# Kernel optimization log

Hardware: AMD Instinct MI355X
Metric: run time of the kernel (lower is better)

The kernel has to match this reference:

```python
import jax, jax.numpy as jnp
import numpy as np

QLEN, MLEN, BSZ, DMODEL, NHEAD, DHEAD, DFF = 1024, 1024, 4, 1024, 16, 64, 4096
KLEN = QLEN + MLEN


def _layernorm(x, g, b, eps=1e-5):
    mu = jnp.mean(x, axis=-1, keepdims=True)
    var = jnp.var(x, axis=-1, keepdims=True)
    return (x - mu) * jax.lax.rsqrt(var + eps) * g + b


def _rel_shift(x):
    # x: [qlen, klen, bsz, nhead] -- Transformer-XL shift trick
    q, k, b, n = x.shape
    x = jnp.pad(x, ((0, 0), (1, 0), (0, 0), (0, 0)))  # [q, k+1, b, n]
    x = x.reshape(k + 1, q, b, n)[1:]
    return x.reshape(q, k, b, n)


def setup_inputs() -> dict:
    key = jax.random.key(0)
    ks = jax.random.split(key, 16)
    s = 0.02
    inp = {
        "word_embed": jax.random.normal(ks[0], (QLEN, BSZ, DMODEL), jnp.float32),
        "pos_embed": jax.random.normal(ks[1], (KLEN, DMODEL), jnp.float32),
        "bias_q": jax.random.normal(ks[2], (NHEAD, DHEAD), jnp.float32) * s,
        "bias_k": jax.random.normal(ks[3], (NHEAD, DHEAD), jnp.float32) * s,
        "memories": jax.random.normal(ks[4], (MLEN, BSZ, DMODEL), jnp.float32),
        "W_qkv": jax.random.normal(ks[5], (DMODEL, 3 * NHEAD * DHEAD), jnp.float32) * s,
        "W_r": jax.random.normal(ks[6], (DMODEL, NHEAD * DHEAD), jnp.float32) * s,
        "W_o": jax.random.normal(ks[7], (NHEAD * DHEAD, DMODEL), jnp.float32) * s,
        "ln1_g": jnp.ones((DMODEL,), jnp.float32),
        "ln1_b": jnp.zeros((DMODEL,), jnp.float32),
        "W_ff1": jax.random.normal(ks[8], (DMODEL, DFF), jnp.float32) * s,
        "b_ff1": jnp.zeros((DFF,), jnp.float32),
        "W_ff2": jax.random.normal(ks[9], (DFF, DMODEL), jnp.float32) * s,
        "b_ff2": jnp.zeros((DMODEL,), jnp.float32),
        "ln2_g": jnp.ones((DMODEL,), jnp.float32),
        "ln2_b": jnp.zeros((DMODEL,), jnp.float32),
    }
    # causal mask with memory: position i may attend to j <= i + MLEN; True = masked
    i = jnp.arange(QLEN)[:, None]
    j = jnp.arange(KLEN)[None, :]
    inp["attention_mask"] = j > (i + MLEN)
    return inp


def reference(word_embed, pos_embed, bias_q, bias_k, attention_mask, memories,
              W_qkv, W_r, W_o, ln1_g, ln1_b, W_ff1, b_ff1, W_ff2, b_ff2, ln2_g, ln2_b):
    scale = 1.0 / np.sqrt(DHEAD)
    cat = jnp.concatenate([memories, word_embed], axis=0)  # [klen, b, d]
    w_heads = cat @ W_qkv  # [klen, b, 3*n*dh]
    q, k, v = jnp.split(w_heads, 3, axis=-1)
    q = q[-QLEN:].reshape(QLEN, BSZ, NHEAD, DHEAD)
    k = k.reshape(KLEN, BSZ, NHEAD, DHEAD)
    v = v.reshape(KLEN, BSZ, NHEAD, DHEAD)
    r = (pos_embed @ W_r).reshape(KLEN, NHEAD, DHEAD)

    AC = jnp.einsum('ibnd,jbnd->ijbn', q + bias_q, k)          # content term
    BD = jnp.einsum('ibnd,jnd->ijbn', q + bias_k, r)           # position term
    BD = _rel_shift(BD)
    score = (AC + BD) * scale
    score = jnp.where(attention_mask[:, :, None, None], -1e30, score)
    prob = jax.nn.softmax(score, axis=1)
    attn_vec = jnp.einsum('ijbn,jbnd->ibnd', prob, v).reshape(QLEN, BSZ, NHEAD * DHEAD)
    attn_out = attn_vec @ W_o
    out = _layernorm(word_embed + attn_out, ln1_g, ln1_b)       # post-LN (pre_lnorm=False)

    core = jax.nn.relu(out @ W_ff1 + b_ff1) @ W_ff2 + b_ff2
    return _layernorm(out + core, ln2_g, ln2_b)
```

## Files before the change

kernel.cpp:

```cpp
#include <hip/hip_runtime.h>


typedef __bf16 bf16x8 __attribute__((ext_vector_type(8)));
typedef float f32x4 __attribute__((ext_vector_type(4)));

#define DEVI __device__ __forceinline__

DEVI unsigned short f2bf(float f) {
  union { float f; unsigned int u; } v;
  v.f = f;
  unsigned int u = v.u;
  u += 0x7fffu + ((u >> 16) & 1u);
  return (unsigned short)(u >> 16);
}

DEVI void load16(const unsigned short* g, unsigned short* l) {
  __builtin_amdgcn_global_load_lds(
      (const __attribute__((address_space(1))) unsigned int*)g,
      (__attribute__((address_space(3))) unsigned int*)l, 16, 0, 0);
}

__global__ __launch_bounds__(256) void cvt_all_kernel(
    const float* __restrict__ mem, const float* __restrict__ we,
    const float* __restrict__ pe, unsigned short* __restrict__ catb,
    unsigned short* __restrict__ posb) {
  const int b = blockIdx.x;
  const float* in;
  unsigned short* out;
  int idx;
  if (b < 4096) {
    in = mem; out = catb; idx = b;
  } else if (b < 8192) {
    in = we; out = catb + (size_t)4096 * 1024; idx = b - 4096;
  } else {
    in = pe; out = posb; idx = b - 8192;
  }
  const size_t i = ((size_t)idx * 256 + threadIdx.x) * 4;
  float4 v = *(const float4*)(in + i);
  ushort4 o;
  o.x = f2bf(v.x);
  o.y = f2bf(v.y);
  o.z = f2bf(v.z);
  o.w = f2bf(v.w);
  *(ushort4*)(out + i) = o;
}

__global__ __launch_bounds__(256) void transpose_all_kernel(
    const float* __restrict__ Wqkv, const float* __restrict__ Wr,
    const float* __restrict__ Wo, const float* __restrict__ Wff1,
    const float* __restrict__ Wff2, unsigned short* __restrict__ Tqkv,
    unsigned short* __restrict__ Tr, unsigned short* __restrict__ To,
    unsigned short* __restrict__ Tff1, unsigned short* __restrict__ Tff2) {
  __shared__ unsigned short t[64][72];
  const int b = blockIdx.x;
  const float* in;
  unsigned short* out;
  int ntx, R, C, local;
  if (b < 768) {
    in = Wqkv; out = Tqkv; ntx = 48; R = 1024; C = 3072; local = b;
  } else if (b < 1024) {
    in = Wr; out = Tr; ntx = 16; R = 1024; C = 1024; local = b - 768;
  } else if (b < 1280) {
    in = Wo; out = To; ntx = 16; R = 1024; C = 1024; local = b - 1024;
  } else if (b < 2304) {
    in = Wff1; out = Tff1; ntx = 64; R = 1024; C = 4096; local = b - 1280;
  } else {
    in = Wff2; out = Tff2; ntx = 16; R = 4096; C = 1024; local = b - 2304;
  }
  const int r0 = (local / ntx) * 64, c0 = (local % ntx) * 64;
  const int tid = threadIdx.x;
#pragma unroll
  for (int it = 0; it < 4; ++it) {
    int f = tid + 256 * it;
    int r = f >> 4;
    int c4 = (f & 15) << 2;
    float4 v = *(const float4*)(in + (size_t)(r0 + r) * C + c0 + c4);
    t[c4 + 0][r] = f2bf(v.x);
    t[c4 + 1][r] = f2bf(v.y);
    t[c4 + 2][r] = f2bf(v.z);
    t[c4 + 3][r] = f2bf(v.w);
  }
  __syncthreads();
#pragma unroll
  for (int it = 0; it < 4; ++it) {
    int f = tid + 256 * it;
    int cc = f >> 4;
    int r4 = (f & 15) << 2;
    ushort4 o;
    o.x = t[cc][r4 + 0];
    o.y = t[cc][r4 + 1];
    o.z = t[cc][r4 + 2];
    o.w = t[cc][r4 + 3];
    *(ushort4*)(out + (size_t)(c0 + cc) * R + r0 + r4) = o;
  }
}

struct GemmArgs {
  const unsigned short* A;
  const unsigned short* Bt;
  int Ks;
  int M, N, K;
  const float* p0;
  const float* p1;
  const float* resid;
  float* outF;
  unsigned short* o0;
  unsigned short* o1;
  unsigned short* o2;
  unsigned short* o3;
  int relu;
  int partial;
};

constexpr int BM = 128, BK = 64;

template <int EPI, int WN = 4>
__global__ __launch_bounds__(256, 4) void gemm_kernel(GemmArgs ga) {
  constexpr int BN_ = WN * 32;
  __shared__ __align__(16) unsigned short As[BM * BK];
  __shared__ __align__(16) unsigned short Bs[BN_ * BK];

  int m0, n0;
  if constexpr (EPI == 0) {
    const int flat = blockIdx.x;
    int mt_, nt_;
    if (flat < 1024) {
      mt_ = flat >> 4;
      nt_ = 8 + (flat & 15);
    } else {
      const int f2 = flat - 1024;
      mt_ = 32 + (f2 >> 3);
      nt_ = f2 & 7;
    }
    m0 = mt_ * 128;
    n0 = nt_ * 128;
  } else {
    n0 = blockIdx.x * BN_;
    m0 = blockIdx.y * BM;
  }
  const int bz = blockIdx.z;
  const int tid = threadIdx.x;
  const int lane = tid & 63;
  const int wv = tid >> 6;
  const int l15 = lane & 15;
  const int quad = lane >> 4;
  const int wm = wv & 1, wn = wv >> 1;
  const int K = ga.K;
  const int Ks = ga.Ks;
  const int r8 = lane >> 3;
  const int sc = (lane & 7) ^ r8;

  const f32x4 fzero = {0.f, 0.f, 0.f, 0.f};
  f32x4 acc[4][WN];
#pragma unroll
  for (int i = 0; i < 4; ++i)
#pragma unroll
    for (int j = 0; j < WN; ++j) acc[i][j] = fzero;

  const unsigned short* Ab =
      ga.A + (size_t)(m0 + 32 * wv + r8) * K + sc * 8 + (size_t)bz * Ks;
  const unsigned short* Bb =
      ga.Bt + (size_t)(n0 + (BN_ / 4) * wv + r8) * K + sc * 8 + (size_t)bz * Ks;
  const int h7 = l15 & 7;

  for (int k0 = 0; k0 < Ks; k0 += BK) {
    __syncthreads();
#pragma unroll
    for (int it = 0; it < 4; ++it)
      load16(Ab + (size_t)(8 * it) * K + k0, &As[(32 * wv + 8 * it) * 64]);
#pragma unroll
    for (int it = 0; it < BN_ / 32; ++it)
      load16(Bb + (size_t)(8 * it) * K + k0, &Bs[((BN_ / 4) * wv + 8 * it) * 64]);
    __syncthreads();
#pragma unroll
    for (int ks = 0; ks < 2; ++ks) {
      bf16x8 af[4], bg[WN];
#pragma unroll
      for (int mt = 0; mt < 4; ++mt)
        af[mt] = *(const bf16x8*)&As[(wm * 64 + mt * 16 + l15) * 64 +
                                     (((ks * 4 + quad) ^ h7) * 8)];
#pragma unroll
      for (int nt = 0; nt < WN; ++nt)
        bg[nt] = *(const bf16x8*)&Bs[(wn * (WN * 16) + nt * 16 + l15) * 64 +
                                     (((ks * 4 + quad) ^ h7) * 8)];
#pragma unroll
      for (int mt = 0; mt < 4; ++mt)
#pragma unroll
        for (int nt = 0; nt < WN; ++nt)
          acc[mt][nt] =
              __builtin_amdgcn_mfma_f32_16x16x32_bf16(af[mt], bg[nt], acc[mt][nt], 0, 0, 0);
    }
  }

#pragma unroll
  for (int mt = 0; mt < 4; ++mt) {
#pragma unroll
    for (int nt = 0; nt < WN; ++nt) {
#pragma unroll
      for (int r = 0; r < 4; ++r) {
        const int row = m0 + wm * 64 + mt * 16 + quad * 4 + r;
        const int col = n0 + wn * (WN * 16) + nt * 16 + l15;
        float val = acc[mt][nt][r];
        if constexpr (EPI == 0) {
          const int seq = row >> 2, b = row & 3;
          if (col < 1024) {
            if (seq >= 1024) {
              const int nh = col >> 6, d = col & 63;
              const size_t o = ((size_t)((b * 16 + nh) * 1024 + (seq - 1024))) * 64 + d;
              ga.o0[o] = f2bf(val + ga.p0[col]);
              ga.o1[o] = f2bf(val + ga.p1[col]);
            }
          } else if (col < 2048) {
            const int c = col - 1024, nh = c >> 6, d = c & 63, bn = b * 16 + nh;
            const size_t o = (size_t)bn * 131072 +
                             (size_t)(((seq >> 4) * 2 + (d >> 5)) * 512) +
                             ((((d >> 3) & 3) * 16 + (seq & 15)) * 8) + (d & 7);
            ga.o2[o] = f2bf(val);
          } else {
            const int c = col - 2048, nh = c >> 6, d = c & 63, bn = b * 16 + nh;
            const size_t o = (size_t)bn * 131072 + (size_t)((seq >> 7) * 8192) +
                             ((((seq >> 5) & 3) * 4 + (d >> 4)) * 512) +
                             ((((seq >> 3) & 3) * 16 + (d & 15)) * 8) + (seq & 7);
            ga.o3[o] = f2bf(val);
          }
        } else if constexpr (EPI == 1) {
          const int nh = col >> 6, d = col & 63, t = row;
          const size_t o = (size_t)nh * 131072 +
                           (size_t)(((t >> 4) * 2 + (d >> 5)) * 512) +
                           ((((d >> 3) & 3) * 16 + (t & 15)) * 8) + (d & 7);
          ga.o0[o] = f2bf(val);
        } else {
          if (ga.partial) {
            ga.outF[(size_t)bz * ((size_t)ga.M * ga.N) + (size_t)row * ga.N + col] = val;
          } else {
            if (ga.p0) val += ga.p0[col];
            if (ga.resid) val += ga.resid[(size_t)row * ga.N + col];
            if (ga.relu) val = fmaxf(val, 0.f);
            if (ga.outF) ga.outF[(size_t)row * ga.N + col] = val;
            if (ga.o0) ga.o0[(size_t)row * ga.N + col] = f2bf(val);
          }
        }
      }
    }
  }
}

constexpr int P_LD = 136;
constexpr float CEXP = 0.18033688f;

__global__ __launch_bounds__(256, 4) void attn_kernel(
    const unsigned short* __restrict__ QQ, const unsigned short* __restrict__ QK,
    const unsigned short* __restrict__ Kf, const unsigned short* __restrict__ Vf,
    const unsigned short* __restrict__ Rf, unsigned short* __restrict__ AVb) {
  __shared__ __align__(16) unsigned short p_s[4][16 * P_LD];

  const int tid = threadIdx.x;
  const int lane = tid & 63;
  const int wv = tid >> 6;
  const int l15 = lane & 15;
  const int quad = lane >> 4;
  const int bn = blockIdx.x;
  const int iw = (blockIdx.y * 4 + wv) * 16;
  const int nh = bn & 15;
  const int bb = bn >> 4;
  unsigned short* pw = &p_s[wv][0];

  const unsigned short* kf = Kf + (size_t)bn * 131072;
  const unsigned short* vf = Vf + (size_t)bn * 131072;
  const unsigned short* rf = Rf + (size_t)nh * 131072;

  const size_t qoff = (size_t)bn * (1024 * 64) + (size_t)(iw + l15) * 64;
  const bf16x8 qq0 = *(const bf16x8*)(QQ + qoff + quad * 8);
  const bf16x8 qq1 = *(const bf16x8*)(QQ + qoff + 32 + quad * 8);
  const bf16x8 qk0 = *(const bf16x8*)(QK + qoff + quad * 8);
  const bf16x8 qk1 = *(const bf16x8*)(QK + qoff + 32 + quad * 8);

  const f32x4 fzero = {0.f, 0.f, 0.f, 0.f};
  f32x4 o_acc[4];
#pragma unroll
  for (int i = 0; i < 4; ++i) o_acc[i] = fzero;
  float lsum[4] = {0.f, 0.f, 0.f, 0.f};

  const int lane8 = lane * 8;
  const int jmax = iw + 15 + 1024;
  for (int j0 = 0; j0 <= jmax; j0 += 128) {
    const int t16b = (j0 >> 4) + 63 - (iw >> 4);
    f32x4 bd[9];
#pragma unroll
    for (int ct = 0; ct < 9; ++ct) {
      int tg = t16b + ct;
      tg = (tg < 127) ? tg : 127;
      const unsigned short* rb = rf + (size_t)(tg * 1024) + lane8;
      bf16x8 b0 = *(const bf16x8*)rb;
      bf16x8 b1 = *(const bf16x8*)(rb + 512);
      f32x4 c = fzero;
      c = __builtin_amdgcn_mfma_f32_16x16x32_bf16(qk0, b0, c, 0, 0, 0);
      c = __builtin_amdgcn_mfma_f32_16x16x32_bf16(qk1, b1, c, 0, 0, 0);
      bd[ct] = c;
    }

    const int ntb = j0 >> 4;
    f32x4 sv[8];
#pragma unroll
    for (int nt = 0; nt < 8; ++nt) {
      const unsigned short* kb = kf + (size_t)((ntb + nt) * 1024) + lane8;
      bf16x8 b0 = *(const bf16x8*)kb;
      bf16x8 b1 = *(const bf16x8*)(kb + 512);
      f32x4 c = fzero;
      c = __builtin_amdgcn_mfma_f32_16x16x32_bf16(qq0, b0, c, 0, 0, 0);
      c = __builtin_amdgcn_mfma_f32_16x16x32_bf16(qq1, b1, c, 0, 0, 0);
      sv[nt] = c;
    }

#pragma unroll
    for (int r = 0; r < 4; ++r) {
      const int il = quad * 4 + r;
      const int u = l15 + 15 - il;
      const int srcl = (lane & 48) | (u & 15);
      float w[9];
#pragma unroll
      for (int ct = 0; ct < 9; ++ct) w[ct] = __shfl(bd[ct][r], srcl, 64);
      const int ig = iw + il;
#pragma unroll
      for (int nt = 0; nt < 8; ++nt) {
        const float bdv = (u & 16) ? w[nt + 1] : w[nt];
        const int jg = j0 + nt * 16 + l15;
        float p = exp2f((sv[nt][r] + bdv) * CEXP);
        p = (jg > ig + 1024) ? 0.f : p;
        lsum[r] += p;
        pw[il * P_LD + nt * 16 + l15] = f2bf(p);
      }
    }

    const unsigned short* vb = vf + (size_t)((j0 >> 7) * 8192) + lane8;
#pragma unroll
    for (int ks = 0; ks < 4; ++ks) {
      bf16x8 ap = *(const bf16x8*)&pw[l15 * P_LD + ks * 32 + quad * 8];
#pragma unroll
      for (int nto = 0; nto < 4; ++nto) {
        bf16x8 bv = *(const bf16x8*)(vb + (ks * 4 + nto) * 512);
        o_acc[nto] = __builtin_amdgcn_mfma_f32_16x16x32_bf16(ap, bv, o_acc[nto], 0, 0, 0);
      }
    }
  }

  float linv[4];
#pragma unroll
  for (int r = 0; r < 4; ++r) {
    float l = lsum[r];
    l += __shfl_xor(l, 1, 64);
    l += __shfl_xor(l, 2, 64);
    l += __shfl_xor(l, 4, 64);
    l += __shfl_xor(l, 8, 64);
    linv[r] = 1.f / l;
  }
#pragma unroll
  for (int nto = 0; nto < 4; ++nto) {
#pragma unroll
    for (int r = 0; r < 4; ++r) {
      const int ig = iw + quad * 4 + r;
      const int d = nto * 16 + l15;
      const float val = o_acc[nto][r] * linv[r];
      AVb[(size_t)(ig * 4 + bb) * 1024 + nh * 64 + d] = f2bf(val);
    }
  }
}

__global__ __launch_bounds__(256) void ln_sum_kernel(
    const float* __restrict__ x0, const float* __restrict__ x1,
    const float* __restrict__ bias, const float* __restrict__ resid,
    const float* __restrict__ g, const float* __restrict__ bta,
    float* __restrict__ outF, unsigned short* __restrict__ outB) {
  const int row = blockIdx.x;
  const int tid = threadIdx.x;
  const size_t off = (size_t)row * 1024 + tid * 4;
  float4 v = *(const float4*)(x0 + off);
  const float4 w = *(const float4*)(x1 + off);
  v.x += w.x; v.y += w.y; v.z += w.z; v.w += w.w;
  if (bias) {
    const float4 b = *(const float4*)(bias + tid * 4);
    v.x += b.x; v.y += b.y; v.z += b.z; v.w += b.w;
  }
  if (resid) {
    const float4 rr = *(const float4*)(resid + off);
    v.x += rr.x; v.y += rr.y; v.z += rr.z; v.w += rr.w;
  }
  float s = v.x + v.y + v.z + v.w;
  float ss = v.x * v.x + v.y * v.y + v.z * v.z + v.w * v.w;
#pragma unroll
  for (int off2 = 1; off2 < 64; off2 <<= 1) {
    s += __shfl_xor(s, off2, 64);
    ss += __shfl_xor(ss, off2, 64);
  }
  __shared__ float red[8];
  const int wv = tid >> 6;
  if ((tid & 63) == 0) {
    red[wv] = s;
    red[4 + wv] = ss;
  }
  __syncthreads();
  s = red[0] + red[1] + red[2] + red[3];
  ss = red[4] + red[5] + red[6] + red[7];
  const float mu = s * (1.f / 1024.f);
  const float var = ss * (1.f / 1024.f) - mu * mu;
  const float rs = rsqrtf(var + 1e-5f);
  const float vv[4] = {v.x, v.y, v.z, v.w};
#pragma unroll
  for (int u = 0; u < 4; ++u) {
    const int c = tid * 4 + u;
    const float y = (vv[u] - mu) * rs * g[c] + bta[c];
    if (outF) outF[(size_t)row * 1024 + c] = y;
    if (outB) outB[(size_t)row * 1024 + c] = f2bf(y);
  }
}

extern "C" void kernel_launch(void* const* d_in, const int* in_sizes, int n_in,
                              void* d_out, int out_size, void* d_ws, size_t ws_size,
                              hipStream_t stream) {
  (void)in_sizes; (void)n_in; (void)out_size; (void)ws_size;
  const float* word_embed = (const float*)d_in[0];
  const float* pos_embed = (const float*)d_in[1];
  const float* bias_q = (const float*)d_in[2];
  const float* bias_k = (const float*)d_in[3];
  const float* memories = (const float*)d_in[4];
  const float* W_qkv = (const float*)d_in[5];
  const float* W_r = (const float*)d_in[6];
  const float* W_o = (const float*)d_in[7];
  const float* ln1_g = (const float*)d_in[8];
  const float* ln1_b = (const float*)d_in[9];
  const float* W_ff1 = (const float*)d_in[10];
  const float* b_ff1 = (const float*)d_in[11];
  const float* W_ff2 = (const float*)d_in[12];
  const float* b_ff2 = (const float*)d_in[13];
  const float* ln2_g = (const float*)d_in[14];
  const float* ln2_b = (const float*)d_in[15];
  float* out = (float*)d_out;

  char* ws = (char*)d_ws;
  unsigned short* QQ = (unsigned short*)(ws + 0);
  unsigned short* QK = (unsigned short*)(ws + 8388608);
  unsigned short* Kf = (unsigned short*)(ws + 16777216);
  unsigned short* Vf = (unsigned short*)(ws + 50331648);
  unsigned short* Rf = (unsigned short*)(ws + 67108864);
  unsigned short* AVb = (unsigned short*)(ws + 71303168);
  float* OUT1 = (float*)(ws + 96468992);
  unsigned short* OUT1b = (unsigned short*)(ws + 113246208);
  unsigned short* Wqkv_t = (unsigned short*)(ws + 121634816);
  unsigned short* Wr_t = (unsigned short*)(ws + 127926272);
  unsigned short* Wo_t = (unsigned short*)(ws + 130023424);
  unsigned short* Wff1_t = (unsigned short*)(ws + 132120576);
  unsigned short* Wff2_t = (unsigned short*)(ws + 140509184);
  unsigned short* Catb = (unsigned short*)(ws + 79691776);
  unsigned short* Posb = (unsigned short*)(ws + 96468992);
  unsigned short* H = (unsigned short*)(ws + 0);
  float* Pwo = (float*)(ws + 33554432);
  float* Pff = (float*)(ws + 50331648);

  const dim3 blk(256);

  cvt_all_kernel<<<10240, blk, 0, stream>>>(memories, word_embed, pos_embed, Catb, Posb);
  transpose_all_kernel<<<3328, blk, 0, stream>>>(W_qkv, W_r, W_o, W_ff1, W_ff2,
                                                 Wqkv_t, Wr_t, Wo_t, Wff1_t, Wff2_t);

  {
    GemmArgs a{};
    a.A = Catb;
    a.Bt = Wqkv_t;
    a.M = 8192; a.N = 3072; a.K = 1024; a.Ks = 1024;
    a.p0 = bias_q; a.p1 = bias_k;
    a.o0 = QQ; a.o1 = QK; a.o2 = Kf; a.o3 = Vf;
    gemm_kernel<0><<<dim3(1280), blk, 0, stream>>>(a);
  }
  {
    GemmArgs a{};
    a.A = Posb;
    a.Bt = Wr_t;
    a.M = 2048; a.N = 1024; a.K = 1024; a.Ks = 1024;
    a.o0 = Rf;
    gemm_kernel<1, 1><<<dim3(32, 16), blk, 0, stream>>>(a);
  }

  attn_kernel<<<dim3(64, 16), blk, 0, stream>>>(QQ, QK, Kf, Vf, Rf, AVb);

  {
    GemmArgs a{};
    a.A = AVb;
    a.Bt = Wo_t;
    a.M = 4096; a.N = 1024; a.K = 1024; a.Ks = 512;
    a.outF = Pwo;
    a.partial = 1;
    gemm_kernel<2, 2><<<dim3(16, 32, 2), blk, 0, stream>>>(a);
  }
  ln_sum_kernel<<<4096, blk, 0, stream>>>(Pwo, Pwo + (size_t)4096 * 1024, nullptr,
                                          word_embed, ln1_g, ln1_b, OUT1, OUT1b);

  {
    GemmArgs a{};
    a.A = OUT1b;
    a.Bt = Wff1_t;
    a.M = 4096; a.N = 4096; a.K = 1024; a.Ks = 1024;
    a.p0 = b_ff1;
    a.relu = 1;
    a.o0 = H;
    gemm_kernel<2><<<dim3(32, 32), blk, 0, stream>>>(a);
  }
  {
    GemmArgs a{};
    a.A = H;
    a.Bt = Wff2_t;
    a.M = 4096; a.N = 1024; a.K = 4096; a.Ks = 2048;
    a.outF = Pff;
    a.partial = 1;
    gemm_kernel<2, 2><<<dim3(16, 32, 2), blk, 0, stream>>>(a);
  }
  ln_sum_kernel<<<4096, blk, 0, stream>>>(Pff, Pff + (size_t)4096 * 1024, b_ff2,
                                          OUT1, ln2_g, ln2_b, out, nullptr);
}
```

Before: 612.1 us.

## Add double-buffered LDS GEMM kernel for narrow-N GEMMs

Adds a gemm_db kernel that keeps two LDS buffers for A and B tiles and issues the next K-tile's global-to-LDS loads before computing on the current one. This needs only one barrier per iteration instead of the single-buffer load/sync/compute/sync sequence. It is used for the positional projection, the W_o GEMM and the FF2 GEMM, all of which have small N tiles. The epilogue is factored into a shared helper. Doubling LDS per block may reduce occupancy, and the in-flight loads may race with reads if the async LDS load ordering is not guaranteed.

```diff
diff --git a/kernel.cpp b/kernel.cpp
--- a/kernel.cpp
+++ b/kernel.cpp
@@ -112,6 +112,49 @@
   int partial;
 };
 
+template <int EPI>
+DEVI void epi_store(const GemmArgs& ga, int bz, int row, int col, float val) {
+  if constexpr (EPI == 0) {
+    const int seq = row >> 2, b = row & 3;
+    if (col < 1024) {
+      if (seq >= 1024) {
+        const int nh = col >> 6, d = col & 63;
+        const size_t o = ((size_t)((b * 16 + nh) * 1024 + (seq - 1024))) * 64 + d;
+        ga.o0[o] = f2bf(val + ga.p0[col]);
+        ga.o1[o] = f2bf(val + ga.p1[col]);
+      }
+    } else if (col < 2048) {
+      const int c = col - 1024, nh = c >> 6, d = c & 63, bn = b * 16 + nh;
+      const size_t o = (size_t)bn * 131072 +
+                       (size_t)(((seq >> 4) * 2 + (d >> 5)) * 512) +
+                       ((((d >> 3) & 3) * 16 + (seq & 15)) * 8) + (d & 7);
+      ga.o2[o] = f2bf(val);
+    } else {
+      const int c = col - 2048, nh = c >> 6, d = c & 63, bn = b * 16 + nh;
+      const size_t o = (size_t)bn * 131072 + (size_t)((seq >> 7) * 8192) +
+                       ((((seq >> 5) & 3) * 4 + (d >> 4)) * 512) +
+                       ((((seq >> 3) & 3) * 16 + (d & 15)) * 8) + (seq & 7);
+      ga.o3[o] = f2bf(val);
+    }
+  } else if constexpr (EPI == 1) {
+    const int nh = col >> 6, d = col & 63, t = row;
+    const size_t o = (size_t)nh * 131072 +
+                     (size_t)(((t >> 4) * 2 + (d >> 5)) * 512) +
+                     ((((d >> 3) & 3) * 16 + (t & 15)) * 8) + (d & 7);
+    ga.o0[o] = f2bf(val);
+  } else {
+    if (ga.partial) {
+      ga.outF[(size_t)bz * ((size_t)ga.M * ga.N) + (size_t)row * ga.N + col] = val;
+    } else {
+      if (ga.p0) val += ga.p0[col];
+      if (ga.resid) val += ga.resid[(size_t)row * ga.N + col];
+      if (ga.relu) val = fmaxf(val, 0.f);
+      if (ga.outF) ga.outF[(size_t)row * ga.N + col] = val;
+      if (ga.o0) ga.o0[(size_t)row * ga.N + col] = f2bf(val);
+    }
+  }
+}
+
 constexpr int BM = 128, BK = 64;
 
 template <int EPI, int WN = 4>
@@ -193,56 +236,97 @@
   }
 
 #pragma unroll
-  for (int mt = 0; mt < 4; ++mt) {
-#pragma unroll
-    for (int nt = 0; nt < WN; ++nt) {
+  for (int mt = 0; mt < 4; ++mt)
+#pragma unroll
+    for (int nt = 0; nt < WN; ++nt)
 #pragma unroll
       for (int r = 0; r < 4; ++r) {
         const int row = m0 + wm * 64 + mt * 16 + quad * 4 + r;
         const int col = n0 + wn * (WN * 16) + nt * 16 + l15;
-        float val = acc[mt][nt][r];
-        if constexpr (EPI == 0) {
-          const int seq = row >> 2, b = row & 3;
-          if (col < 1024) {
-            if (seq >= 1024) {
-              const int nh = col >> 6, d = col & 63;
-              const size_t o = ((size_t)((b * 16 + nh) * 1024 + (seq - 1024))) * 64 + d;
-              ga.o0[o] = f2bf(val + ga.p0[col]);
-              ga.o1[o] = f2bf(val + ga.p1[col]);
-            }
-          } else if (col < 2048) {
-            const int c = col - 1024, nh = c >> 6, d = c & 63, bn = b * 16 + nh;
-            const size_t o = (size_t)bn * 131072 +
-                             (size_t)(((seq >> 4) * 2 + (d >> 5)) * 512) +
-                             ((((d >> 3) & 3) * 16 + (seq & 15)) * 8) + (d & 7);
-            ga.o2[o] = f2bf(val);
-          } else {
-            const int c = col - 2048, nh = c >> 6, d = c & 63, bn = b * 16 + nh;
-            const size_t o = (size_t)bn * 131072 + (size_t)((seq >> 7) * 8192) +
-                             ((((seq >> 5) & 3) * 4 + (d >> 4)) * 512) +
-                             ((((seq >> 3) & 3) * 16 + (d & 15)) * 8) + (seq & 7);
-            ga.o3[o] = f2bf(val);
-          }
-        } else if constexpr (EPI == 1) {
-          const int nh = col >> 6, d = col & 63, t = row;
-          const size_t o = (size_t)nh * 131072 +
-                           (size_t)(((t >> 4) * 2 + (d >> 5)) * 512) +
-                           ((((d >> 3) & 3) * 16 + (t & 15)) * 8) + (d & 7);
-          ga.o0[o] = f2bf(val);
-        } else {
-          if (ga.partial) {
-            ga.outF[(size_t)bz * ((size_t)ga.M * ga.N) + (size_t)row * ga.N + col] = val;
-          } else {
-            if (ga.p0) val += ga.p0[col];
-            if (ga.resid) val += ga.resid[(size_t)row * ga.N + col];
-            if (ga.relu) val = fmaxf(val, 0.f);
-            if (ga.outF) ga.outF[(size_t)row * ga.N + col] = val;
-            if (ga.o0) ga.o0[(size_t)row * ga.N + col] = f2bf(val);
-          }
-        }
+        epi_store<EPI>(ga, bz, row, col, acc[mt][nt][r]);
       }
-    }
-  }
+}
+
+template <int EPI, int WN = 2>
+__global__ __launch_bounds__(256, 4) void gemm_db(GemmArgs ga) {
+  constexpr int BN_ = WN * 32;
+  __shared__ __align__(16) unsigned short As[2][BM * BK];
+  __shared__ __align__(16) unsigned short Bs[2][BN_ * BK];
+
+  const int n0 = blockIdx.x * BN_;
+  const int m0 = blockIdx.y * BM;
+  const int bz = blockIdx.z;
+  const int tid = threadIdx.x;
+  const int lane = tid & 63;
+  const int wv = tid >> 6;
+  const int l15 = lane & 15;
+  const int quad = lane >> 4;
+  const int wm = wv & 1, wn = wv >> 1;
+  const int K = ga.K;
+  const int Ks = ga.Ks;
+  const int r8 = lane >> 3;
+  const int sc = (lane & 7) ^ r8;
+  const int h7 = l15 & 7;
+
+  const f32x4 fzero = {0.f, 0.f, 0.f, 0.f};
+  f32x4 acc[4][WN];
+#pragma unroll
+  for (int i = 0; i < 4; ++i)
+#pragma unroll
+    for (int j = 0; j < WN; ++j) acc[i][j] = fzero;
+
+  const unsigned short* Ab =
+      ga.A + (size_t)(m0 + 32 * wv + r8) * K + sc * 8 + (size_t)bz * Ks;
+  const unsigned short* Bb =
+      ga.Bt + (size_t)(n0 + (BN_ / 4) * wv + r8) * K + sc * 8 + (size_t)bz * Ks;
+
+  auto stage = [&](int k0, int bi) {
+#pragma unroll
+    for (int it = 0; it < 4; ++it)
+      load16(Ab + (size_t)(8 * it) * K + k0, &As[bi][(32 * wv + 8 * it) * 64]);
+#pragma unroll
+    for (int it = 0; it < BN_ / 32; ++it)
+      load16(Bb + (size_t)(8 * it) * K + k0, &Bs[bi][((BN_ / 4) * wv + 8 * it) * 64]);
+  };
+
+  stage(0, 0);
+  __syncthreads();
+
+  int buf = 0;
+  for (int k0 = 0; k0 < Ks; k0 += BK) {
+    if (k0 + BK < Ks) stage(k0 + BK, buf ^ 1);
+#pragma unroll
+    for (int ks = 0; ks < 2; ++ks) {
+      bf16x8 af[4], bg[WN];
+#pragma unroll
+      for (int mt = 0; mt < 4; ++mt)
+        af[mt] = *(const bf16x8*)&As[buf][(wm * 64 + mt * 16 + l15) * 64 +
+                                         (((ks * 4 + quad) ^ h7) * 8)];
+#pragma unroll
+      for (int nt = 0; nt < WN; ++nt)
+        bg[nt] = *(const bf16x8*)&Bs[buf][(wn * (WN * 16) + nt * 16 + l15) * 64 +
+                                          (((ks * 4 + quad) ^ h7) * 8)];
+#pragma unroll
+      for (int mt = 0; mt < 4; ++mt)
+#pragma unroll
+        for (int nt = 0; nt < WN; ++nt)
+          acc[mt][nt] =
+              __builtin_amdgcn_mfma_f32_16x16x32_bf16(af[mt], bg[nt], acc[mt][nt], 0, 0, 0);
+    }
+    __syncthreads();
+    buf ^= 1;
+  }
+
+#pragma unroll
+  for (int mt = 0; mt < 4; ++mt)
+#pragma unroll
+    for (int nt = 0; nt < WN; ++nt)
+#pragma unroll
+      for (int r = 0; r < 4; ++r) {
+        const int row = m0 + wm * 64 + mt * 16 + quad * 4 + r;
+        const int col = n0 + wn * (WN * 16) + nt * 16 + l15;
+        epi_store<EPI>(ga, bz, row, col, acc[mt][nt][r]);
+      }
 }
 
 constexpr int P_LD = 136;
@@ -477,7 +561,7 @@
     a.Bt = Wr_t;
     a.M = 2048; a.N = 1024; a.K = 1024; a.Ks = 1024;
     a.o0 = Rf;
-    gemm_kernel<1, 1><<<dim3(32, 16), blk, 0, stream>>>(a);
+    gemm_db<1, 1><<<dim3(32, 16), blk, 0, stream>>>(a);
   }
 
   attn_kernel<<<dim3(64, 16), blk, 0, stream>>>(QQ, QK, Kf, Vf, Rf, AVb);
@@ -489,7 +573,7 @@
     a.M = 4096; a.N = 1024; a.K = 1024; a.Ks = 512;
     a.outF = Pwo;
     a.partial = 1;
-    gemm_kernel<2, 2><<<dim3(16, 32, 2), blk, 0, stream>>>(a);
+    gemm_db<2, 2><<<dim3(16, 32, 2), blk, 0, stream>>>(a);
   }
   ln_sum_kernel<<<4096, blk, 0, stream>>>(Pwo, Pwo + (size_t)4096 * 1024, nullptr,
                                           word_embed, ln1_g, ln1_b, OUT1, OUT1b);
@@ -511,7 +595,7 @@
     a.M = 4096; a.N = 1024; a.K = 4096; a.Ks = 2048;
     a.outF = Pff;
     a.partial = 1;
-    gemm_kernel<2, 2><<<dim3(16, 32, 2), blk, 0, stream>>>(a);
+    gemm_db<2, 2><<<dim3(16, 32, 2), blk, 0, stream>>>(a);
   }
   ln_sum_kernel<<<4096, blk, 0, stream>>>(Pff, Pff + (size_t)4096 * 1024, b_ff2,
                                           OUT1, ln2_g, ln2_b, out, nullptr);
```

Result: slower. 634.6 us (+3.7%).
